# Performance work log

Hardware: AMD Instinct MI355X
Metric: run time of the kernel (lower is better)

The kernel has to match this reference:

```python
import jax, jax.numpy as jnp
import numpy as np

HEADS = 32


def _conv1x1(x, w, b):
    # x: (B, Cin, H, W); w: (Cout, Cin); 1x1 conv == per-pixel GEMM
    return jnp.einsum('bchw,oc->bohw', x, w) + b[None, :, None, None]


def _grid_sample2d_zeros(value, grid):
    # value: (N, C, H, W); grid: (N, H, W, 2), normalized coords in [-1, 1],
    # grid[..., 0] = x (width axis), grid[..., 1] = y (height axis).
    # Bilinear, align_corners=True, zeros padding applied per dimension.
    N, C, H, W = value.shape
    ix = (grid[..., 0] + 1.0) * (W - 1) * 0.5
    iy = (grid[..., 1] + 1.0) * (H - 1) * 0.5
    x0 = jnp.floor(ix)
    y0 = jnp.floor(iy)
    dx = ix - x0  # (N, H, W)
    dy = iy - y0
    x0i = x0.astype(jnp.int32)
    y0i = y0.astype(jnp.int32)
    x1i = x0i + 1
    y1i = y0i + 1

    def gather(yi, xi):
        valid = ((xi >= 0) & (xi < W) & (yi >= 0) & (yi < H))
        xc = jnp.clip(xi, 0, W - 1)
        yc = jnp.clip(yi, 0, H - 1)
        g = jax.vmap(lambda v, y, x: v[:, y, x])(value, yc, xc)  # (N, C, H, W)
        return g * valid[:, None, :, :].astype(value.dtype)

    out = (gather(y0i, x0i) * ((1.0 - dx) * (1.0 - dy))[:, None]
           + gather(y0i, x1i) * (dx * (1.0 - dy))[:, None]
           + gather(y1i, x0i) * ((1.0 - dx) * dy)[:, None]
           + gather(y1i, x1i) * (dx * dy)[:, None])
    return out


def _base_grid(H, W, dtype):
    ys = jnp.linspace(-1.0, 1.0, H, dtype=dtype)
    xs = jnp.linspace(-1.0, 1.0, W, dtype=dtype)
    gy, gx = jnp.meshgrid(ys, xs, indexing='ij')
    return jnp.stack([gx, gy], axis=-1)  # (H, W, 2)


def setup_inputs() -> dict:
    key = jax.random.key(0)
    k = jax.random.split(key, 8)
    B, Cin, Cout, H, W = 4, 256, 256, 128, 128
    u = jax.random.normal(k[0], (B, Cin, H, W), dtype=jnp.float32)
    s_in = 1.0 / np.sqrt(Cin)
    s_out = 1.0 / np.sqrt(Cout)
    w1 = jax.random.normal(k[1], (Cout, Cin), dtype=jnp.float32) * s_in
    b1 = jax.random.normal(k[2], (Cout,), dtype=jnp.float32) * 0.01
    w2 = jax.random.normal(k[3], (2 * HEADS, Cout), dtype=jnp.float32) * (0.1 * s_out)
    b2 = jax.random.normal(k[4], (2 * HEADS,), dtype=jnp.float32) * 0.01
    wv = jax.random.normal(k[5], (Cout, Cin), dtype=jnp.float32) * s_in
    bv = jax.random.normal(k[6], (Cout,), dtype=jnp.float32) * 0.01
    return {"u": u, "w1": w1, "b1": b1, "w2": w2, "b2": b2, "wv": wv, "bv": bv}


def reference(u, w1, b1, w2, b2, wv, bv):
    B, Cin, H, W = u.shape
    # flow_head: 1x1 conv -> ReLU -> 1x1 conv producing n_dims*heads channels
    h = jax.nn.relu(_conv1x1(u, w1, b1))
    flow = _conv1x1(h, w2, b2)          # (B, heads*2, H, W)
    value = _conv1x1(u, wv, bv)         # (B, Cout, H, W)
    Ci = value.shape[1] // HEADS
    # 'B (heads dir) H W -> (B heads) H W dir'
    flow = flow.reshape(B, HEADS, 2, H, W).transpose(0, 1, 3, 4, 2)
    flow = flow.reshape(B * HEADS, H, W, 2)
    # 'B (heads C_i) H W -> (B heads) C_i H W'
    value = value.reshape(B * HEADS, Ci, H, W)
    grid = _base_grid(H, W, u.dtype)[None] + flow  # (B*heads, H, W, 2)
    warp = _grid_sample2d_zeros(value, grid)       # (B*heads, Ci, H, W)
    # '(B heads) C_i H W -> B (heads C_i) H W'
    return warp.reshape(B, HEADS * Ci, H, W)
```

## Files before the change

kernel.cpp:

```cpp
#include <hip/hip_runtime.h>
#include <cstddef>

#define HW 16384

typedef short s8v __attribute__((ext_vector_type(8)));
typedef short s4v __attribute__((ext_vector_type(4)));
typedef float f4v __attribute__((ext_vector_type(4)));

__device__ inline short f2b(float x) {
    union { float f; unsigned u; } v; v.f = x;
    unsigned r = v.u + 0x7fff + ((v.u >> 16) & 1);
    return (short)(r >> 16);
}
__device__ inline float b2f(short h) {
    union { unsigned u; float f; } v;
    v.u = ((unsigned)(unsigned short)h) << 16;
    return v.f;
}

__global__ __launch_bounds__(256) void k_prep_w(
    const float* __restrict__ w1, const float* __restrict__ wv,
    const float* __restrict__ w2,
    short* __restrict__ Wthi, short* __restrict__ Wtlo,
    short* __restrict__ w2thi, short* __restrict__ w2tlo)
{
    int tid = blockIdx.x * 256 + threadIdx.x;
    if (tid < 131072) {
        int c = tid >> 14, r = tid & 16383, ch = r >> 5, kk = r & 31;
        float f = (ch < 256) ? w1[ch * 256 + c * 32 + kk]
                             : wv[(ch - 256) * 256 + c * 32 + kk];
        short hi = f2b(f);
        Wthi[tid] = hi;
        if (ch < 256) Wtlo[(c * 256 + ch) * 32 + kk] = f2b(f - b2f(hi));
    } else {
        int o = tid - 131072;
        int c = o >> 11, r = o & 2047, dir = r >> 5, kk = r & 31;
        float f = w2[dir * 256 + c * 32 + kk];
        short hi = f2b(f);
        w2thi[o] = hi;
        w2tlo[o] = f2b(f - b2f(hi));
    }
}

__global__ __launch_bounds__(256, 2) void k_mega(
    const float* __restrict__ u,
    const short* __restrict__ Wthi, const short* __restrict__ Wtlo,
    const short* __restrict__ w2thi, const short* __restrict__ w2tlo,
    const float* __restrict__ b1, const float* __restrict__ bv,
    const float* __restrict__ b2,
    unsigned short* __restrict__ vbuf, float* __restrict__ flow)
{
    __shared__ __attribute__((aligned(16))) char smem[69632];
    short* T1h = (short*)smem;
    short* T1l = T1h + 4352;
    short* T2h = (short*)(smem + 17408);
    short* T2l = T2h + 4608;
    short* vt  = (short*)smem;
    short* hhi = (short*)smem;
    short* hlo = (short*)(smem + 34816);

    const int t = threadIdx.x;
    const int l = t & 63;
    const int w = t >> 6;
    const int lr = l & 15;
    const int quad = l >> 4;
    const int quad8 = quad * 8;
    const int pt = blockIdx.x * 64;
    const int b  = pt >> 14;
    const int p0 = pt & 16383;
    const float* ub = u + (size_t)b * 256 * HW + p0;
    const int pxB = 16 * w + lr;

    f4v acc_h[4][4], acc_v[4][4];
    #pragma unroll
    for (int i = 0; i < 4; ++i)
        #pragma unroll
        for (int j = 0; j < 4; ++j) {
            acc_h[i][j] = (f4v){0.f, 0.f, 0.f, 0.f};
            acc_v[i][j] = (f4v){0.f, 0.f, 0.f, 0.f};
        }

    float4 cur[4];
    #pragma unroll
    for (int i = 0; i < 4; ++i) {
        int idx = t + 256 * i;
        int ch = idx >> 4, px4 = (idx & 15) * 4;
        cur[i] = *reinterpret_cast<const float4*>(ub + (size_t)ch * HW + px4);
    }

    for (int pair = 0; pair < 4; ++pair) {
        #pragma unroll
        for (int i = 0; i < 4; ++i) {
            int idx = t + 256 * i;
            int ch = idx >> 4, px4 = (idx & 15) * 4;
            float4 v = cur[i];
            short h0 = f2b(v.x), h1 = f2b(v.y), h2 = f2b(v.z), h3 = f2b(v.w);
            s4v hv = {h0, h1, h2, h3};
            s4v lv = {f2b(v.x - b2f(h0)), f2b(v.y - b2f(h1)),
                      f2b(v.z - b2f(h2)), f2b(v.w - b2f(h3))};
            *reinterpret_cast<s4v*>(T1h + ch * 68 + px4) = hv;
            *reinterpret_cast<s4v*>(T1l + ch * 68 + px4) = lv;
        }
        __syncthreads();
        #pragma unroll
        for (int part = 0; part < 2; ++part) {
            const short* src = part ? T1l : T1h;
            short* dst = part ? T2l : T2h;
            #pragma unroll
            for (int j = 0; j < 4; ++j) {
                int k4 = (l >> 4) + 4 * j;
                s4v v = { src[(4 * k4 + 0) * 68 + pxB],
                          src[(4 * k4 + 1) * 68 + pxB],
                          src[(4 * k4 + 2) * 68 + pxB],
                          src[(4 * k4 + 3) * 68 + pxB] };
                *reinterpret_cast<s4v*>(dst + pxB * 72 + 4 * k4) = v;
            }
        }
        __syncthreads();
        if (pair < 3) {
            #pragma unroll
            for (int i = 0; i < 4; ++i) {
                int idx = t + 256 * i;
                int ch = idx >> 4, px4 = (idx & 15) * 4;
                cur[i] = *reinterpret_cast<const float4*>(
                    ub + (size_t)((pair + 1) * 64 + ch) * HW + px4);
            }
        }
        #pragma unroll
        for (int s = 0; s < 2; ++s) {
            int c = pair * 2 + s;
            s8v bh4[4], bl4[4];
            #pragma unroll
            for (int j = 0; j < 4; ++j) {
                bh4[j] = *reinterpret_cast<const s8v*>(T2h + (16 * j + lr) * 72 + s * 32 + quad8);
                bl4[j] = *reinterpret_cast<const s8v*>(T2l + (16 * j + lr) * 72 + s * 32 + quad8);
            }
            #pragma unroll
            for (int i = 0; i < 4; ++i) {
                const size_t wb = ((size_t)c * 512 + 64 * w + 16 * i + lr) * 32 + quad8;
                s8v ahi = *reinterpret_cast<const s8v*>(Wthi + wb);
                s8v av  = *reinterpret_cast<const s8v*>(Wthi + wb + 256 * 32);
                s8v alo = *reinterpret_cast<const s8v*>(
                    Wtlo + ((size_t)c * 256 + 64 * w + 16 * i + lr) * 32 + quad8);
                #pragma unroll
                for (int j = 0; j < 4; ++j) {
                    acc_h[i][j] = __builtin_amdgcn_mfma_f32_16x16x32_bf16(ahi, bh4[j], acc_h[i][j], 0, 0, 0);
                    acc_h[i][j] = __builtin_amdgcn_mfma_f32_16x16x32_bf16(ahi, bl4[j], acc_h[i][j], 0, 0, 0);
                    acc_h[i][j] = __builtin_amdgcn_mfma_f32_16x16x32_bf16(alo, bh4[j], acc_h[i][j], 0, 0, 0);
                    acc_v[i][j] = __builtin_amdgcn_mfma_f32_16x16x32_bf16(av,  bh4[j], acc_v[i][j], 0, 0, 0);
                }
            }
        }
        __syncthreads();
    }

    #pragma unroll
    for (int i = 0; i < 4; ++i) {
        float4 bias = *reinterpret_cast<const float4*>(bv + 64 * w + 16 * i + 4 * quad);
        #pragma unroll
        for (int j = 0; j < 4; ++j) {
            int px = 16 * j + lr;
            s4v pk = { f2b(acc_v[i][j][0] + bias.x), f2b(acc_v[i][j][1] + bias.y),
                       f2b(acc_v[i][j][2] + bias.z), f2b(acc_v[i][j][3] + bias.w) };
            *reinterpret_cast<s4v*>(vt + px * 272 + 64 * w + 16 * i + 4 * quad) = pk;
        }
    }
    __syncthreads();
    {
        int px = t >> 2, ch0 = (t & 3) * 64;
        size_t pixg = (size_t)(b << 14) + p0 + px;
        #pragma unroll
        for (int e = 0; e < 8; ++e) {
            s8v vv = *reinterpret_cast<const s8v*>(vt + px * 272 + ch0 + 8 * e);
            *reinterpret_cast<s8v*>(vbuf + pixg * 256 + ch0 + 8 * e) = vv;
        }
    }
    __syncthreads();

    #pragma unroll
    for (int i = 0; i < 4; ++i) {
        float4 bias = *reinterpret_cast<const float4*>(b1 + 64 * w + 16 * i + 4 * quad);
        #pragma unroll
        for (int j = 0; j < 4; ++j) {
            int px = 16 * j + lr;
            float v0 = fmaxf(acc_h[i][j][0] + bias.x, 0.f);
            float v1 = fmaxf(acc_h[i][j][1] + bias.y, 0.f);
            float v2 = fmaxf(acc_h[i][j][2] + bias.z, 0.f);
            float v3 = fmaxf(acc_h[i][j][3] + bias.w, 0.f);
            short h0 = f2b(v0), h1 = f2b(v1), h2 = f2b(v2), h3 = f2b(v3);
            s4v hv = {h0, h1, h2, h3};
            s4v lv = {f2b(v0 - b2f(h0)), f2b(v1 - b2f(h1)),
                      f2b(v2 - b2f(h2)), f2b(v3 - b2f(h3))};
            int chb = 64 * w + 16 * i + 4 * quad;
            *reinterpret_cast<s4v*>(hhi + px * 272 + chb) = hv;
            *reinterpret_cast<s4v*>(hlo + px * 272 + chb) = lv;
        }
    }
    __syncthreads();

    f4v acc_f[4];
    #pragma unroll
    for (int j = 0; j < 4; ++j) acc_f[j] = (f4v){0.f, 0.f, 0.f, 0.f};
    #pragma unroll
    for (int c = 0; c < 8; ++c) {
        const size_t wb = ((size_t)c * 64 + 16 * w + lr) * 32 + quad8;
        s8v ahi = *reinterpret_cast<const s8v*>(w2thi + wb);
        s8v alo = *reinterpret_cast<const s8v*>(w2tlo + wb);
        #pragma unroll
        for (int j = 0; j < 4; ++j) {
            int px = 16 * j + lr;
            s8v bhh = *reinterpret_cast<const s8v*>(hhi + px * 272 + c * 32 + quad8);
            s8v bll = *reinterpret_cast<const s8v*>(hlo + px * 272 + c * 32 + quad8);
            acc_f[j] = __builtin_amdgcn_mfma_f32_16x16x32_bf16(ahi, bhh, acc_f[j], 0, 0, 0);
            acc_f[j] = __builtin_amdgcn_mfma_f32_16x16x32_bf16(ahi, bll, acc_f[j], 0, 0, 0);
            acc_f[j] = __builtin_amdgcn_mfma_f32_16x16x32_bf16(alo, bhh, acc_f[j], 0, 0, 0);
        }
    }
    float4 b2v = *reinterpret_cast<const float4*>(b2 + 16 * w + 4 * quad);
    #pragma unroll
    for (int r = 0; r < 4; ++r) {
        int dir = 16 * w + 4 * quad + r;
        float bias = (r == 0) ? b2v.x : (r == 1) ? b2v.y : (r == 2) ? b2v.z : b2v.w;
        #pragma unroll
        for (int j = 0; j < 4; ++j)
            flow[((size_t)b * 64 + dir) * HW + p0 + 16 * j + lr] = acc_f[j][r] + bias;
    }
}

__global__ __launch_bounds__(256) void k_warp(
    const float* __restrict__ flow, const unsigned short* __restrict__ vbuf,
    float* __restrict__ out)
{
    const int g = blockIdx.x * 256 + threadIdx.x;
    const int p = g & 16383;
    const int n = g >> 14;
    const int b = n >> 5;
    const int head = n & 31;
    const int y = p >> 7;
    const int x = p & 127;

    float fx = flow[((size_t)b * 64 + 2 * head + 0) * HW + p];
    float fy = flow[((size_t)b * 64 + 2 * head + 1) * HW + p];
    float ix = (float)x + fx * 63.5f;
    float iy = (float)y + fy * 63.5f;

    float x0f = floorf(ix), y0f = floorf(iy);
    float dx = ix - x0f, dy = iy - y0f;
    int x0 = (int)x0f, y0 = (int)y0f;
    int x1 = x0 + 1,   y1 = y0 + 1;

    bool vx0 = (x0 >= 0) & (x0 < 128);
    bool vx1 = (x1 >= 0) & (x1 < 128);
    bool vy0 = (y0 >= 0) & (y0 < 128);
    bool vy1 = (y1 >= 0) & (y1 < 128);
    int x0c = min(max(x0, 0), 127), x1c = min(max(x1, 0), 127);
    int y0c = min(max(y0, 0), 127), y1c = min(max(y1, 0), 127);

    float w00 = (1.f - dx) * (1.f - dy) * ((vx0 & vy0) ? 1.f : 0.f);
    float w10 = dx * (1.f - dy)        * ((vx1 & vy0) ? 1.f : 0.f);
    float w01 = (1.f - dx) * dy        * ((vx0 & vy1) ? 1.f : 0.f);
    float w11 = dx * dy                * ((vx1 & vy1) ? 1.f : 0.f);

    const unsigned short* vb = vbuf + ((size_t)(b << 14)) * 256 + head * 8;
    s8v v00 = *reinterpret_cast<const s8v*>(vb + (size_t)(y0c * 128 + x0c) * 256);
    s8v v10 = *reinterpret_cast<const s8v*>(vb + (size_t)(y0c * 128 + x1c) * 256);
    s8v v01 = *reinterpret_cast<const s8v*>(vb + (size_t)(y1c * 128 + x0c) * 256);
    s8v v11 = *reinterpret_cast<const s8v*>(vb + (size_t)(y1c * 128 + x1c) * 256);

    float* ob = out + ((size_t)b * 256 + head * 8) * HW + p;
    #pragma unroll
    for (int ci = 0; ci < 8; ++ci) {
        float v = w00 * b2f(v00[ci]) + w10 * b2f(v10[ci])
                + w01 * b2f(v01[ci]) + w11 * b2f(v11[ci]);
        ob[(size_t)ci * HW] = v;
    }
}

extern "C" void kernel_launch(void* const* d_in, const int* in_sizes, int n_in,
                              void* d_out, int out_size, void* d_ws, size_t ws_size,
                              hipStream_t stream) {
    const float* u  = (const float*)d_in[0];
    const float* w1 = (const float*)d_in[1];
    const float* b1 = (const float*)d_in[2];
    const float* w2 = (const float*)d_in[3];
    const float* b2 = (const float*)d_in[4];
    const float* wv = (const float*)d_in[5];
    const float* bv = (const float*)d_in[6];

    char* ws = (char*)d_ws;
    unsigned short* vbuf = (unsigned short*)ws;
    float* flow  = (float*)(ws + 33554432ull);
    short* Wthi  = (short*)(ws + 50331648ull);
    short* Wtlo  = Wthi + 131072;
    short* w2thi = Wtlo + 65536;
    short* w2tlo = w2thi + 16384;
    float* out = (float*)d_out;

    k_prep_w<<<dim3(576),  dim3(256), 0, stream>>>(w1, wv, w2, Wthi, Wtlo, w2thi, w2tlo);
    k_mega  <<<dim3(1024), dim3(256), 0, stream>>>(u, Wthi, Wtlo, w2thi, w2tlo,
                                                   b1, bv, b2, vbuf, flow);
    k_warp  <<<dim3(8192), dim3(256), 0, stream>>>(flow, vbuf, out);
}
```

Baseline: 217.9 us.

## Store value buffer per head, prefetch weights, use lightweight LDS barriers

Result: faster. 198.0 us (-9.1%).

```diff
diff --git a/kernel.cpp b/kernel.cpp
--- a/kernel.cpp
+++ b/kernel.cpp
@@ -16,6 +16,10 @@
     union { unsigned u; float f; } v;
     v.u = ((unsigned)(unsigned short)h) << 16;
     return v.f;
+}
+
+__device__ inline void bar_lgkm() {
+    asm volatile("s_waitcnt lgkmcnt(0)\n\ts_barrier" ::: "memory");
 }
 
 __global__ __launch_bounds__(256) void k_prep_w(
@@ -88,6 +92,14 @@
         cur[i] = *reinterpret_cast<const float4*>(ub + (size_t)ch * HW + px4);
     }
 
+    s8v nx_hi, nx_v, nx_lo;
+    {
+        const size_t wb0 = ((size_t)(64 * w + lr)) * 32 + quad8;
+        nx_hi = *reinterpret_cast<const s8v*>(Wthi + wb0);
+        nx_v  = *reinterpret_cast<const s8v*>(Wthi + wb0 + 256 * 32);
+        nx_lo = *reinterpret_cast<const s8v*>(Wtlo + wb0);
+    }
+
     for (int pair = 0; pair < 4; ++pair) {
         #pragma unroll
         for (int i = 0; i < 4; ++i) {
@@ -101,7 +113,7 @@
             *reinterpret_cast<s4v*>(T1h + ch * 68 + px4) = hv;
             *reinterpret_cast<s4v*>(T1l + ch * 68 + px4) = lv;
         }
-        __syncthreads();
+        bar_lgkm();
         #pragma unroll
         for (int part = 0; part < 2; ++part) {
             const short* src = part ? T1l : T1h;
@@ -116,7 +128,7 @@
                 *reinterpret_cast<s4v*>(dst + pxB * 72 + 4 * k4) = v;
             }
         }
-        __syncthreads();
+        bar_lgkm();
         if (pair < 3) {
             #pragma unroll
             for (int i = 0; i < 4; ++i) {
@@ -137,11 +149,17 @@
             }
             #pragma unroll
             for (int i = 0; i < 4; ++i) {
-                const size_t wb = ((size_t)c * 512 + 64 * w + 16 * i + lr) * 32 + quad8;
-                s8v ahi = *reinterpret_cast<const s8v*>(Wthi + wb);
-                s8v av  = *reinterpret_cast<const s8v*>(Wthi + wb + 256 * 32);
-                s8v alo = *reinterpret_cast<const s8v*>(
-                    Wtlo + ((size_t)c * 256 + 64 * w + 16 * i + lr) * 32 + quad8);
+                s8v ahi = nx_hi, av = nx_v, alo = nx_lo;
+                {
+                    int idx = c * 4 + i + 1;
+                    int ni = idx & 3;
+                    int nc = (idx >> 2) & 7;
+                    const size_t wb = ((size_t)nc * 512 + 64 * w + 16 * ni + lr) * 32 + quad8;
+                    nx_hi = *reinterpret_cast<const s8v*>(Wthi + wb);
+                    nx_v  = *reinterpret_cast<const s8v*>(Wthi + wb + 256 * 32);
+                    nx_lo = *reinterpret_cast<const s8v*>(
+                        Wtlo + ((size_t)nc * 256 + 64 * w + 16 * ni + lr) * 32 + quad8);
+                }
                 #pragma unroll
                 for (int j = 0; j < 4; ++j) {
                     acc_h[i][j] = __builtin_amdgcn_mfma_f32_16x16x32_bf16(ahi, bh4[j], acc_h[i][j], 0, 0, 0);
@@ -151,7 +169,7 @@
                 }
             }
         }
-        __syncthreads();
+        bar_lgkm();
     }
 
     #pragma unroll
@@ -165,17 +183,20 @@
             *reinterpret_cast<s4v*>(vt + px * 272 + 64 * w + 16 * i + 4 * quad) = pk;
         }
     }
-    __syncthreads();
+    bar_lgkm();
     {
-        int px = t >> 2, ch0 = (t & 3) * 64;
-        size_t pixg = (size_t)(b << 14) + p0 + px;
+        int px = t >> 2;
+        int h0 = (t & 3) * 8;
+        size_t pix = (size_t)p0 + px;
         #pragma unroll
         for (int e = 0; e < 8; ++e) {
-            s8v vv = *reinterpret_cast<const s8v*>(vt + px * 272 + ch0 + 8 * e);
-            *reinterpret_cast<s8v*>(vbuf + pixg * 256 + ch0 + 8 * e) = vv;
-        }
-    }
-    __syncthreads();
+            int hh = h0 + e;
+            s8v vv = *reinterpret_cast<const s8v*>(vt + px * 272 + hh * 8);
+            *reinterpret_cast<s8v*>(
+                vbuf + ((((size_t)(b * 32 + hh)) << 14) + pix) * 8) = vv;
+        }
+    }
+    bar_lgkm();
 
     #pragma unroll
     for (int i = 0; i < 4; ++i) {
@@ -196,16 +217,26 @@
             *reinterpret_cast<s4v*>(hlo + px * 272 + chb) = lv;
         }
     }
-    __syncthreads();
+    s8v f_hi, f_lo;
+    {
+        const size_t wb = ((size_t)(16 * w + lr)) * 32 + quad8;
+        f_hi = *reinterpret_cast<const s8v*>(w2thi + wb);
+        f_lo = *reinterpret_cast<const s8v*>(w2tlo + wb);
+    }
+    bar_lgkm();
 
     f4v acc_f[4];
     #pragma unroll
     for (int j = 0; j < 4; ++j) acc_f[j] = (f4v){0.f, 0.f, 0.f, 0.f};
     #pragma unroll
     for (int c = 0; c < 8; ++c) {
-        const size_t wb = ((size_t)c * 64 + 16 * w + lr) * 32 + quad8;
-        s8v ahi = *reinterpret_cast<const s8v*>(w2thi + wb);
-        s8v alo = *reinterpret_cast<const s8v*>(w2tlo + wb);
+        s8v ahi = f_hi, alo = f_lo;
+        {
+            int ncf = (c + 1) & 7;
+            const size_t wb = ((size_t)ncf * 64 + 16 * w + lr) * 32 + quad8;
+            f_hi = *reinterpret_cast<const s8v*>(w2thi + wb);
+            f_lo = *reinterpret_cast<const s8v*>(w2tlo + wb);
+        }
         #pragma unroll
         for (int j = 0; j < 4; ++j) {
             int px = 16 * j + lr;
@@ -261,11 +292,11 @@
     float w01 = (1.f - dx) * dy        * ((vx0 & vy1) ? 1.f : 0.f);
     float w11 = dx * dy                * ((vx1 & vy1) ? 1.f : 0.f);
 
-    const unsigned short* vb = vbuf + ((size_t)(b << 14)) * 256 + head * 8;
-    s8v v00 = *reinterpret_cast<const s8v*>(vb + (size_t)(y0c * 128 + x0c) * 256);
-    s8v v10 = *reinterpret_cast<const s8v*>(vb + (size_t)(y0c * 128 + x1c) * 256);
-    s8v v01 = *reinterpret_cast<const s8v*>(vb + (size_t)(y1c * 128 + x0c) * 256);
-    s8v v11 = *reinterpret_cast<const s8v*>(vb + (size_t)(y1c * 128 + x1c) * 256);
+    const unsigned short* vb = vbuf + (((size_t)n) << 14) * 8;
+    s8v v00 = *reinterpret_cast<const s8v*>(vb + (size_t)(y0c * 128 + x0c) * 8);
+    s8v v10 = *reinterpret_cast<const s8v*>(vb + (size_t)(y0c * 128 + x1c) * 8);
+    s8v v01 = *reinterpret_cast<const s8v*>(vb + (size_t)(y1c * 128 + x0c) * 8);
+    s8v v11 = *reinterpret_cast<const s8v*>(vb + (size_t)(y1c * 128 + x1c) * 8);
 
     float* ob = out + ((size_t)b * 256 + head * 8) * HW + p;
     #pragma unroll
```
